# Performance work log

Hardware: AMD Instinct MI355X
Metric: run time of the kernel (lower is better)

## Reference

```python
import jax, jax.numpy as jnp
import numpy as np

BSZ, SEQ, NVARS = 4, 512, 7
DM, NH, DFF, EL, FACTOR, PRED = 512, 8, 2048, 2, 5, 96
DH = DM // NH


def layer_norm(x, g, b, eps=1e-5):
    mu = jnp.mean(x, -1, keepdims=True)
    var = jnp.mean((x - mu) ** 2, -1, keepdims=True)
    return (x - mu) / jnp.sqrt(var + eps) * g + b


def prob_attention(q, k, v, key, factor=FACTOR):
    # q,k,v: (B,H,L,D); Informer ProbSparse self-attention (non-causal)
    B, H, L, D = q.shape
    Lk = k.shape[2]
    U_part = min(int(factor * np.ceil(np.log(Lk))), Lk)  # sampled keys per query
    u = min(int(factor * np.ceil(np.log(L))), L)         # top queries kept
    idx = jax.random.randint(key, (L, U_part), 0, Lk)
    k_s = k[:, :, idx]                                   # (B,H,L,U,D) gathered keys
    qk_s = jnp.einsum('bhld,bhlud->bhlu', q, k_s)
    M = qk_s.max(-1) - qk_s.sum(-1) / Lk                 # sparsity measure (div by L_K, as in Informer)
    _, top = jax.lax.top_k(M, u)                         # (B,H,u) active query indices
    q_r = jnp.take_along_axis(q, top[..., None], axis=2)  # (B,H,u,D)
    scale = np.float32(1.0 / np.sqrt(D))
    scores = jnp.einsum('bhud,bhkd->bhuk', q_r, k) * scale
    attn = jax.nn.softmax(scores, axis=-1)
    upd = jnp.einsum('bhuk,bhkd->bhud', attn, v)
    # initial context = mean of V for every query; overwrite active queries
    ctx = jnp.broadcast_to(jnp.mean(v, axis=2, keepdims=True), (B, H, L, D))
    bi = jnp.arange(B)[:, None, None]
    hi = jnp.arange(H)[None, :, None]
    return ctx.at[bi, hi, top].set(upd)


def encoder_layer(x, p, key):
    Wq, bq, Wk, bk, Wv, bv, Wo, bo, W1, b1, W2, b2, g1, be1, g2, be2 = p
    B, L, _ = x.shape
    q = (x @ Wq.T + bq).reshape(B, L, NH, DH).transpose(0, 2, 1, 3)
    k = (x @ Wk.T + bk).reshape(B, L, NH, DH).transpose(0, 2, 1, 3)
    v = (x @ Wv.T + bv).reshape(B, L, NH, DH).transpose(0, 2, 1, 3)
    ctx = prob_attention(q, k, v, key)
    out = ctx.transpose(0, 2, 1, 3).reshape(B, L, DM) @ Wo.T + bo
    x = layer_norm(x + out, g1, be1)
    y = jax.nn.gelu(x @ W1.T + b1) @ W2.T + b2
    return layer_norm(x + y, g2, be2)


def _forward(x_enc, w_emb, b_emb, w_pos, Wq, bq, Wk, bk, Wv, bv, Wo, bo,
             W1, b1, W2, b2, g1, be1, g2, be2, gF, bF, Wh, bh):
    B, L, V = x_enc.shape
    emb = x_enc[..., None] * w_emb + b_emb               # (B,L,V,DM)  Linear(1,DM) per scalar
    h = emb.transpose(0, 2, 1, 3).reshape(B * V, L, DM) + w_pos
    base = jax.random.key(42)
    for l in range(EL):
        p = (Wq[l], bq[l], Wk[l], bk[l], Wv[l], bv[l], Wo[l], bo[l],
             W1[l], b1[l], W2[l], b2[l], g1[l], be1[l], g2[l], be2[l])
        h = encoder_layer(h, p, jax.random.fold_in(base, l))
    h = layer_norm(h, gF, bF)
    h = h.reshape(B, V, L * DM)                          # flatten head: nf = SEQ*DM
    out = h @ Wh.T + bh                                  # (B,V,PRED)
    return out.transpose(0, 2, 1)                        # (B,PRED,V)


def setup_inputs() -> dict:
    key = jax.random.key(0)
    ks = jax.random.split(key, 32)
    s = 0.02
    d = {
        'x_enc': jax.random.normal(ks[0], (BSZ, SEQ, NVARS), jnp.float32),
        'w_emb': jax.random.normal(ks[1], (DM,), jnp.float32) * s,
        'b_emb': jnp.zeros((DM,), jnp.float32),
        'w_pos': jax.random.normal(ks[2], (SEQ, DM), jnp.float32) * s,
        'Wq': jax.random.normal(ks[3], (EL, DM, DM), jnp.float32) * s,
        'bq': jnp.zeros((EL, DM), jnp.float32),
        'Wk': jax.random.normal(ks[4], (EL, DM, DM), jnp.float32) * s,
        'bk': jnp.zeros((EL, DM), jnp.float32),
        'Wv': jax.random.normal(ks[5], (EL, DM, DM), jnp.float32) * s,
        'bv': jnp.zeros((EL, DM), jnp.float32),
        'Wo': jax.random.normal(ks[6], (EL, DM, DM), jnp.float32) * s,
        'bo': jnp.zeros((EL, DM), jnp.float32),
        'W1': jax.random.normal(ks[7], (EL, DFF, DM), jnp.float32) * s,
        'b1': jnp.zeros((EL, DFF), jnp.float32),
        'W2': jax.random.normal(ks[8], (EL, DM, DFF), jnp.float32) * s,
        'b2': jnp.zeros((EL, DM), jnp.float32),
        'g1': jnp.ones((EL, DM), jnp.float32),
        'be1': jnp.zeros((EL, DM), jnp.float32),
        'g2': jnp.ones((EL, DM), jnp.float32),
        'be2': jnp.zeros((EL, DM), jnp.float32),
        'gF': jnp.ones((DM,), jnp.float32),
        'bF': jnp.zeros((DM,), jnp.float32),
        'Wh': jax.random.normal(ks[9], (PRED, SEQ * DM), jnp.float32) * 0.002,
        'bh': jnp.zeros((PRED,), jnp.float32),
    }
    return d


def reference(x_enc, w_emb, b_emb, w_pos, Wq, bq, Wk, bk, Wv, bv, Wo, bo,
              W1, b1, W2, b2, g1, be1, g2, be2, gF, bF, Wh, bh):
    return _forward(x_enc, w_emb, b_emb, w_pos, Wq, bq, Wk, bk, Wv, bv, Wo, bo,
                    W1, b1, W2, b2, g1, be1, g2, be2, gF, bF, Wh, bh)
```

## Files before the change

kernel.cpp:

```cpp
#include <hip/hip_runtime.h>
#include <math.h>

#define SEQL 512
#define DMOD 512
#define NHEAD 8
#define DHEAD 64
#define DFFN 2048
#define NBATCH 4
#define NVARS 7
#define NBV 28
#define NBH 224
#define NROWS 14336
#define NSAMP 35
#define NPRED 96
#define SBIG 7340032
#define QKS 1024

typedef short bf16x8 __attribute__((ext_vector_type(8)));
typedef float f32x4 __attribute__((ext_vector_type(4)));

#define GLDS(gptr, lptr) \
  __builtin_amdgcn_global_load_lds((const __attribute__((address_space(1))) void*)(gptr), \
                                   (__attribute__((address_space(3))) void*)(lptr), 16, 0, 0)

__device__ inline unsigned short f2b(float f) {
  unsigned u = __builtin_bit_cast(unsigned, f);
  unsigned r = (u + 0x7FFFu + ((u >> 16) & 1u)) >> 16;
  return (unsigned short)r;
}
__device__ inline float b2f(unsigned short h) {
  return __builtin_bit_cast(float, (unsigned)h << 16);
}

__device__ inline void threefry2x32(unsigned k0, unsigned k1,
                                    unsigned x0, unsigned x1,
                                    unsigned &o0, unsigned &o1) {
  unsigned ks2 = k0 ^ k1 ^ 0x1BD11BDAu;
  unsigned ks[3] = {k0, k1, ks2};
  x0 += k0; x1 += k1;
  const unsigned rot[2][4] = {{13u,15u,26u,6u},{17u,29u,16u,24u}};
  #pragma unroll
  for (int i = 0; i < 5; ++i) {
    #pragma unroll
    for (int j = 0; j < 4; ++j) {
      unsigned r = rot[i & 1][j];
      x0 += x1;
      x1 = (x1 << r) | (x1 >> (32u - r));
      x1 ^= x0;
    }
    x0 += ks[(i + 1) % 3];
    x1 += ks[(i + 2) % 3] + (unsigned)(i + 1);
  }
  o0 = x0; o1 = x1;
}

__global__ void make_idx_kernel(int layer, int* idx) {
  int i = blockIdx.x * 256 + threadIdx.x;
  if (i >= SEQL * NSAMP) return;
  unsigned kl0, kl1, o0, o1;
  threefry2x32(0u, 42u, 0u, (unsigned)layer, kl0, kl1);
  threefry2x32(kl0, kl1, (unsigned)i, (unsigned)(SEQL * NSAMP + i), o0, o1);
  idx[i] = (int)(o1 & 511u);
}

__global__ void embed_kernel(const float* __restrict__ x_enc,
                             const float* __restrict__ w_emb,
                             const float* __restrict__ b_emb,
                             const float* __restrict__ w_pos,
                             float* __restrict__ h,
                             unsigned short* __restrict__ h_hi,
                             unsigned short* __restrict__ h_lo) {
  size_t i = (size_t)blockIdx.x * 256 + threadIdx.x;
  if (i >= (size_t)(SBIG / 4)) return;
  size_t e = i * 4;
  int dm = (int)(e & 511);
  int l  = (int)((e >> 9) & 511);
  int bv = (int)(e >> 18);
  int b = bv / NVARS, v = bv % NVARS;
  float xs = x_enc[((size_t)b * SEQL + l) * NVARS + v];
  float4 we = *(const float4*)(w_emb + dm);
  float4 bb = *(const float4*)(b_emb + dm);
  float4 wp = *(const float4*)(w_pos + (size_t)l * DMOD + dm);
  float4 val;
  val.x = xs * we.x + bb.x + wp.x;
  val.y = xs * we.y + bb.y + wp.y;
  val.z = xs * we.z + bb.z + wp.z;
  val.w = xs * we.w + bb.w + wp.w;
  *(float4*)(h + e) = val;
  ushort4 hi4, lo4;
  hi4.x = f2b(val.x); lo4.x = f2b(val.x - b2f(hi4.x));
  hi4.y = f2b(val.y); lo4.y = f2b(val.y - b2f(hi4.y));
  hi4.z = f2b(val.z); lo4.z = f2b(val.z - b2f(hi4.z));
  hi4.w = f2b(val.w); lo4.w = f2b(val.w - b2f(hi4.w));
  *(ushort4*)(h_hi + e) = hi4;
  *(ushort4*)(h_lo + e) = lo4;
}

__global__ void prep_weights(const float* __restrict__ Wq, const float* __restrict__ Wk,
                             const float* __restrict__ Wv, const float* __restrict__ Wo,
                             const float* __restrict__ W1, const float* __restrict__ W2,
                             unsigned short* __restrict__ Wqk_hi, unsigned short* __restrict__ Wqk_lo,
                             unsigned short* __restrict__ Wv_b, unsigned short* __restrict__ Wo_b,
                             unsigned short* __restrict__ W1_b, unsigned short* __restrict__ W2_b) {
  const int Q4 = 65536;
  int g = blockIdx.x * 256 + threadIdx.x;
  if (g < 2 * Q4) {
    const float* src = g < Q4 ? Wq : Wk;
    unsigned short* hi = Wqk_hi + (g < Q4 ? 0 : DMOD * DMOD);
    unsigned short* lo = Wqk_lo + (g < Q4 ? 0 : DMOD * DMOD);
    int off = (g < Q4 ? g : g - Q4) * 4;
    float4 v = *(const float4*)(src + off);
    ushort4 h4, l4;
    h4.x = f2b(v.x); l4.x = f2b(v.x - b2f(h4.x));
    h4.y = f2b(v.y); l4.y = f2b(v.y - b2f(h4.y));
    h4.z = f2b(v.z); l4.z = f2b(v.z - b2f(h4.z));
    h4.w = f2b(v.w); l4.w = f2b(v.w - b2f(h4.w));
    *(ushort4*)(hi + off) = h4;
    *(ushort4*)(lo + off) = l4;
    return;
  }
  const float* src;
  unsigned short* dst;
  int off;
  if (g < 3 * Q4)      { src = Wv; dst = Wv_b; off = (g - 2 * Q4) * 4; }
  else if (g < 4 * Q4) { src = Wo; dst = Wo_b; off = (g - 3 * Q4) * 4; }
  else if (g < 4 * Q4 + 262144) { src = W1; dst = W1_b; off = (g - 4 * Q4) * 4; }
  else                 { src = W2; dst = W2_b; off = (g - 4 * Q4 - 262144) * 4; }
  float4 v = *(const float4*)(src + off);
  ushort4 o;
  o.x = f2b(v.x); o.y = f2b(v.y); o.z = f2b(v.z); o.w = f2b(v.w);
  *(ushort4*)(dst + off) = o;
}

__global__ __launch_bounds__(256) void gemm_mfma3(const unsigned short* __restrict__ Ah,
                                                  const unsigned short* __restrict__ Al,
                                                  const unsigned short* __restrict__ Bh,
                                                  const unsigned short* __restrict__ Bl,
                                                  const float* __restrict__ bq,
                                                  const float* __restrict__ bk,
                                                  float* __restrict__ C,
                                                  int M, int N, int K, int ldc) {
  __shared__ __align__(16) unsigned short AsH[128 * 64];
  __shared__ __align__(16) unsigned short AsL[128 * 64];
  __shared__ __align__(16) unsigned short BsH[128 * 64];
  __shared__ __align__(16) unsigned short BsL[128 * 64];
  int nwg = gridDim.x * gridDim.y;
  int flat = blockIdx.y * gridDim.x + blockIdx.x;
  int swz = (flat & 7) * (nwg >> 3) + (flat >> 3);
  int bxs = swz % gridDim.x, bys = swz / gridDim.x;
  int bm = bys * 128, bn = bxs * 128;
  int tid = threadIdx.x;
  int wave = tid >> 6, lane = tid & 63;
  int wr = wave >> 1, wc = wave & 1;
  int r16 = lane & 15, kq = lane >> 4;

  f32x4 acc[4][4];
  #pragma unroll
  for (int i = 0; i < 4; ++i)
    #pragma unroll
    for (int j = 0; j < 4; ++j) acc[i][j] = (f32x4){0.f, 0.f, 0.f, 0.f};

  for (int kt = 0; kt < K; kt += 64) {
    __syncthreads();
    #pragma unroll
    for (int i = 0; i < 4; ++i) {
      int c = i * 256 + tid;
      int row = c >> 3, kb = c & 7;
      int kbs = kb ^ (row & 7);
      size_t offA = (size_t)(bm + row) * K + kt + kbs * 8;
      size_t offB = (size_t)(bn + row) * K + kt + kbs * 8;
      int ldst = (i * 256 + (tid & 192)) << 4;
      GLDS(Ah + offA, (char*)AsH + ldst);
      GLDS(Al + offA, (char*)AsL + ldst);
      GLDS(Bh + offB, (char*)BsH + ldst);
      GLDS(Bl + offB, (char*)BsL + ldst);
    }
    __syncthreads();
    #pragma unroll
    for (int ks = 0; ks < 2; ++ks) {
      bf16x8 ah[4], al[4], bh[4], bl[4];
      #pragma unroll
      for (int mi = 0; mi < 4; ++mi) {
        int row = wr * 64 + mi * 16 + r16;
        int addr = ((row << 7) | (ks << 6) | (kq << 4)) ^ ((row & 7) << 4);
        ah[mi] = *(const bf16x8*)((const char*)AsH + addr);
        al[mi] = *(const bf16x8*)((const char*)AsL + addr);
      }
      #pragma unroll
      for (int ni = 0; ni < 4; ++ni) {
        int row = wc * 64 + ni * 16 + r16;
        int addr = ((row << 7) | (ks << 6) | (kq << 4)) ^ ((row & 7) << 4);
        bh[ni] = *(const bf16x8*)((const char*)BsH + addr);
        bl[ni] = *(const bf16x8*)((const char*)BsL + addr);
      }
      #pragma unroll
      for (int mi = 0; mi < 4; ++mi)
        #pragma unroll
        for (int ni = 0; ni < 4; ++ni) {
          acc[mi][ni] = __builtin_amdgcn_mfma_f32_16x16x32_bf16(ah[mi], bh[ni], acc[mi][ni], 0, 0, 0);
          acc[mi][ni] = __builtin_amdgcn_mfma_f32_16x16x32_bf16(ah[mi], bl[ni], acc[mi][ni], 0, 0, 0);
          acc[mi][ni] = __builtin_amdgcn_mfma_f32_16x16x32_bf16(al[mi], bh[ni], acc[mi][ni], 0, 0, 0);
        }
    }
  }
  int crow0 = bm + wr * 64 + (lane >> 4) * 4;
  int ccol0 = bn + wc * 64 + (lane & 15);
  #pragma unroll
  for (int mi = 0; mi < 4; ++mi) {
    #pragma unroll
    for (int ni = 0; ni < 4; ++ni) {
      int col = ccol0 + ni * 16;
      float bvv = col < 512 ? bq[col] : bk[col - 512];
      #pragma unroll
      for (int r = 0; r < 4; ++r) {
        int row = crow0 + mi * 16 + r;
        C[(size_t)row * ldc + col] = acc[mi][ni][r] + bvv;
      }
    }
  }
}

template<int ACT, int OUTBF>
__global__ __launch_bounds__(256) void gemm_mfma(const unsigned short* __restrict__ A,
                                                 const unsigned short* __restrict__ W,
                                                 const float* __restrict__ bias,
                                                 float* __restrict__ Cf,
                                                 unsigned short* __restrict__ Cb,
                                                 int M, int N, int K) {
  __shared__ __align__(16) unsigned short As[2][128 * 64];
  __shared__ __align__(16) unsigned short Bs[2][128 * 64];
  int nwg = gridDim.x * gridDim.y;
  int flat = blockIdx.y * gridDim.x + blockIdx.x;
  int swz = (flat & 7) * (nwg >> 3) + (flat >> 3);
  int bxs = swz % gridDim.x, bys = swz / gridDim.x;
  int bm = bys * 128, bn = bxs * 128;
  int tid = threadIdx.x;
  int wave = tid >> 6, lane = tid & 63;
  int wr = wave >> 1, wc = wave & 1;
  int r16 = lane & 15, kq = lane >> 4;

  f32x4 acc[4][4];
  #pragma unroll
  for (int i = 0; i < 4; ++i)
    #pragma unroll
    for (int j = 0; j < 4; ++j) acc[i][j] = (f32x4){0.f, 0.f, 0.f, 0.f};

#define STAGE_MM(buf, ktv) \
  { \
    for (int i_ = 0; i_ < 4; ++i_) { \
      int c_ = i_ * 256 + tid; \
      int row_ = c_ >> 3, kb_ = c_ & 7; \
      int kbs_ = kb_ ^ (row_ & 7); \
      size_t offA_ = (size_t)(bm + row_) * K + (ktv) + kbs_ * 8; \
      size_t offB_ = (size_t)(bn + row_) * K + (ktv) + kbs_ * 8; \
      int ldst_ = (i_ * 256 + (tid & 192)) << 4; \
      GLDS(A + offA_, (char*)As[buf] + ldst_); \
      GLDS(W + offB_, (char*)Bs[buf] + ldst_); \
    } \
  }

  int nkt = K >> 6;
  STAGE_MM(0, 0);
  __syncthreads();
  for (int t = 0; t < nkt; ++t) {
    int cur = t & 1;
    if (t + 1 < nkt) STAGE_MM(cur ^ 1, (t + 1) << 6);
    const char* Ab = (const char*)As[cur];
    const char* Bb = (const char*)Bs[cur];
    #pragma unroll
    for (int ks = 0; ks < 2; ++ks) {
      bf16x8 afr[4], bfr[4];
      #pragma unroll
      for (int mi = 0; mi < 4; ++mi) {
        int row = wr * 64 + mi * 16 + r16;
        int addr = ((row << 7) | (ks << 6) | (kq << 4)) ^ ((row & 7) << 4);
        afr[mi] = *(const bf16x8*)(Ab + addr);
      }
      #pragma unroll
      for (int ni = 0; ni < 4; ++ni) {
        int row = wc * 64 + ni * 16 + r16;
        int addr = ((row << 7) | (ks << 6) | (kq << 4)) ^ ((row & 7) << 4);
        bfr[ni] = *(const bf16x8*)(Bb + addr);
      }
      #pragma unroll
      for (int mi = 0; mi < 4; ++mi)
        #pragma unroll
        for (int ni = 0; ni < 4; ++ni)
          acc[mi][ni] = __builtin_amdgcn_mfma_f32_16x16x32_bf16(afr[mi], bfr[ni], acc[mi][ni], 0, 0, 0);
    }
    __syncthreads();
  }
#undef STAGE_MM

  int crow0 = bm + wr * 64 + (lane >> 4) * 4;
  int ccol0 = bn + wc * 64 + (lane & 15);
  #pragma unroll
  for (int mi = 0; mi < 4; ++mi) {
    #pragma unroll
    for (int ni = 0; ni < 4; ++ni) {
      int col = ccol0 + ni * 16;
      float bvv = bias[col];
      #pragma unroll
      for (int r = 0; r < 4; ++r) {
        int row = crow0 + mi * 16 + r;
        float v = acc[mi][ni][r] + bvv;
        if (ACT) {
          float x = v;
          float u = x * __builtin_fmaf(0.044715f * x, x, 1.0f);
          float tme = __expf(-1.5957691216057308f * u);
          v = x * __builtin_amdgcn_rcpf(1.0f + tme);
        }
        if (OUTBF) Cb[(size_t)row * N + col] = f2b(v);
        else       Cf[(size_t)row * N + col] = v;
      }
    }
  }
}

__global__ __launch_bounds__(512) void m2_kernel(const float* __restrict__ QK,
                                                 const int* __restrict__ idx,
                                                 float* __restrict__ Mout) {
  int bh = blockIdx.x;
  int bv = bh >> 3, head = bh & 7;
  int tid = threadIdx.x;
  __shared__ float Ks[512 * 64];
  const float* base = QK + (size_t)bv * (SEQL * QKS);
  for (int c = tid; c < 512 * 16; c += 512) {
    int l = c >> 4, db = c & 15;
    float4 v = *(const float4*)(base + (size_t)l * QKS + 512 + head * 64 + db * 4);
    *(float4*)(Ks + l * 64 + ((db ^ (l & 15)) << 2)) = v;
  }
  float q[64];
  const float* qp = base + (size_t)tid * QKS + head * 64;
  #pragma unroll
  for (int d4 = 0; d4 < 64; d4 += 4) {
    float4 qv = *(const float4*)(qp + d4);
    q[d4 + 0] = qv.x; q[d4 + 1] = qv.y; q[d4 + 2] = qv.z; q[d4 + 3] = qv.w;
  }
  __syncthreads();
  const int* ip = idx + tid * NSAMP;
  float mx = -INFINITY, sm = 0.f;
  for (int u = 0; u < NSAMP; ++u) {
    int kidx = ip[u];
    const float* kr = Ks + kidx * 64;
    int x = kidx & 15;
    float s = 0.f;
    #pragma unroll
    for (int db = 0; db < 16; ++db) {
      float4 kv = *(const float4*)(kr + ((db ^ x) << 2));
      s += q[db * 4 + 0] * kv.x + q[db * 4 + 1] * kv.y
         + q[db * 4 + 2] * kv.z + q[db * 4 + 3] * kv.w;
    }
    mx = fmaxf(mx, s);
    sm += s;
  }
  Mout[(size_t)bh * SEQL + tid] = mx - sm * (1.0f / 512.0f);
}

__global__ __launch_bounds__(256) void topk_kernel(const float* __restrict__ Mv,
                                                   int* __restrict__ top) {
  int bh = blockIdx.x;
  int tid = threadIdx.x;
  __shared__ float vals[512];
  __shared__ float rv[256];
  __shared__ int ri[256];
  vals[tid]       = Mv[(size_t)bh * SEQL + tid];
  vals[tid + 256] = Mv[(size_t)bh * SEQL + tid + 256];
  __syncthreads();
  for (int t = 0; t < NSAMP; ++t) {
    float v0 = vals[tid], v1 = vals[tid + 256];
    float bvv; int bii;
    if (v0 >= v1) { bvv = v0; bii = tid; } else { bvv = v1; bii = tid + 256; }
    rv[tid] = bvv; ri[tid] = bii;
    __syncthreads();
    for (int s = 128; s > 0; s >>= 1) {
      if (tid < s) {
        float ov = rv[tid + s]; int oi = ri[tid + s];
        if (ov > rv[tid] || (ov == rv[tid] && oi < ri[tid])) { rv[tid] = ov; ri[tid] = oi; }
      }
      __syncthreads();
    }
    if (tid == 0) { top[bh * NSAMP + t] = ri[0]; vals[ri[0]] = -INFINITY; }
    __syncthreads();
  }
}

__global__ __launch_bounds__(256) void vmean_kernel(const unsigned short* __restrict__ Vb,
                                                    float* __restrict__ vmean) {
  int bv = blockIdx.x;
  int t = threadIdx.x;
  const unsigned short* vb = Vb + (size_t)bv * (SEQL * DMOD) + t * 2;
  float s0 = 0.f, s1 = 0.f;
  #pragma unroll 4
  for (int l = 0; l < SEQL; ++l) {
    unsigned u = *(const unsigned*)(vb + (size_t)l * DMOD);
    s0 += b2f((unsigned short)(u & 0xffffu));
// ... 87 lines not shown
      for (int j = 0; j < 8; ++j) {
        int l = (wv * 8 + j) * 16 + r16;
        #pragma unroll
        for (int r = 0; r < 4; ++r) {
          int u = m * 16 + kq * 4 + r;
          int byte = ((u << 10) | (l << 1)) ^ ((u & 7) << 4);
          *(unsigned short*)((char*)P + byte) = f2b(acc[m][j][r]);
        }
      }
  }
  __syncthreads();

  for (int c = tid; c < 512 * 8; c += 256) {
    int l = c >> 3, dq = c & 7;
    bf16x8 v8 = *(const bf16x8*)(vbase + (size_t)l * DMOD + dq * 8);
    #pragma unroll
    for (int j = 0; j < 8; ++j) {
      int d = dq * 8 + j;
      int byte = ((d << 10) | (l << 1)) ^ ((d & 7) << 4);
      *(unsigned short*)((char*)KV + byte) = (unsigned short)v8[j];
    }
  }
  for (int u = wv; u < NSAMP; u += 4) {
    int byte = ((u << 10) | (lane << 4)) ^ ((u & 7) << 4);
    bf16x8 sv = *(const bf16x8*)((const char*)P + byte);
    float s[8];
    #pragma unroll
    for (int j = 0; j < 8; ++j) s[j] = b2f((unsigned short)sv[j]);
    float mx = s[0];
    #pragma unroll
    for (int j = 1; j < 8; ++j) mx = fmaxf(mx, s[j]);
    #pragma unroll
    for (int off = 32; off > 0; off >>= 1) mx = fmaxf(mx, __shfl_xor(mx, off));
    float e[8], sm = 0.f;
    #pragma unroll
    for (int j = 0; j < 8; ++j) { e[j] = __expf(s[j] - mx); sm += e[j]; }
    #pragma unroll
    for (int off = 32; off > 0; off >>= 1) sm += __shfl_xor(sm, off);
    float inv = 1.0f / sm;
    bf16x8 pv;
    #pragma unroll
    for (int j = 0; j < 8; ++j) pv[j] = (short)f2b(e[j] * inv);
    *(bf16x8*)((char*)P + byte) = pv;
  }
  __syncthreads();

  {
    f32x4 acc2[3];
    #pragma unroll
    for (int m = 0; m < 3; ++m) acc2[m] = (f32x4){0.f, 0.f, 0.f, 0.f};
    for (int kst = 0; kst < 16; ++kst) {
      int vrow = wv * 16 + r16;
      int baddr = ((vrow << 10) | (kst << 6) | (kq << 4)) ^ ((vrow & 7) << 4);
      bf16x8 bfr = *(const bf16x8*)((const char*)KV + baddr);
      #pragma unroll
      for (int m = 0; m < 3; ++m) {
        int prow = m * 16 + r16;
        int aaddr = ((prow << 10) | (kst << 6) | (kq << 4)) ^ ((prow & 7) << 4);
        bf16x8 afr2 = *(const bf16x8*)((const char*)P + aaddr);
        acc2[m] = __builtin_amdgcn_mfma_f32_16x16x32_bf16(afr2, bfr, acc2[m], 0, 0, 0);
      }
    }
    int d = wv * 16 + r16;
    #pragma unroll
    for (int m = 0; m < 3; ++m)
      #pragma unroll
      for (int r = 0; r < 4; ++r) {
        int u = m * 16 + kq * 4 + r;
        if (u < NSAMP) {
          size_t off = (size_t)bv * (SEQL * DMOD) + (size_t)topi[u] * DMOD + head * 64 + d;
          ctxb[off] = f2b(acc2[m][r]);
        }
      }
  }
}

template<int BMODE, int OUT>
__global__ __launch_bounds__(256) void add_ln(const float* __restrict__ a,
                                              const unsigned short* __restrict__ b,
                                              const float* __restrict__ g,
                                              const float* __restrict__ be,
                                              float* __restrict__ out,
                                              unsigned short* __restrict__ outb,
                                              unsigned short* __restrict__ outh,
                                              unsigned short* __restrict__ outl) {
  int row = blockIdx.x * 2 + (threadIdx.x >> 7);
  int t = threadIdx.x & 127;
  int wave = threadIdx.x >> 6;
  int lane = threadIdx.x & 63;
  size_t base = (size_t)row * DMOD + t * 4;
  float4 x = *(const float4*)(a + base);
  if (BMODE == 2) {
    ushort4 r4 = *(const ushort4*)(b + base);
    x.x += b2f(r4.x); x.y += b2f(r4.y); x.z += b2f(r4.z); x.w += b2f(r4.w);
  }
  float s1 = x.x + x.y + x.z + x.w;
  float s2 = x.x * x.x + x.y * x.y + x.z * x.z + x.w * x.w;
  #pragma unroll
  for (int off = 32; off > 0; off >>= 1) {
    s1 += __shfl_xor(s1, off);
    s2 += __shfl_xor(s2, off);
  }
  __shared__ float sh[8];
  if (lane == 0) { sh[wave * 2] = s1; sh[wave * 2 + 1] = s2; }
  __syncthreads();
  int mate = wave ^ 1;
  s1 += sh[mate * 2];
  s2 += sh[mate * 2 + 1];
  float mu = s1 * (1.0f / 512.0f);
  float var = s2 * (1.0f / 512.0f) - mu * mu;
  float rstd = rsqrtf(var + 1e-5f);
  float4 gg = *(const float4*)(g + t * 4);
  float4 bb = *(const float4*)(be + t * 4);
  float4 o;
  o.x = (x.x - mu) * rstd * gg.x + bb.x;
  o.y = (x.y - mu) * rstd * gg.y + bb.y;
  o.z = (x.z - mu) * rstd * gg.z + bb.z;
  o.w = (x.w - mu) * rstd * gg.w + bb.w;
  *(float4*)(out + base) = o;
  if (OUT == 1) {
    ushort4 ob;
    ob.x = f2b(o.x); ob.y = f2b(o.y); ob.z = f2b(o.z); ob.w = f2b(o.w);
    *(ushort4*)(outb + base) = ob;
  }
  if (OUT == 2) {
    ushort4 hi4, lo4;
    hi4.x = f2b(o.x); lo4.x = f2b(o.x - b2f(hi4.x));
    hi4.y = f2b(o.y); lo4.y = f2b(o.y - b2f(hi4.y));
    hi4.z = f2b(o.z); lo4.z = f2b(o.z - b2f(hi4.z));
    hi4.w = f2b(o.w); lo4.w = f2b(o.w - b2f(hi4.w));
    *(ushort4*)(outh + base) = hi4;
    *(ushort4*)(outl + base) = lo4;
  }
}

__global__ __launch_bounds__(256) void head_partial_mfma(const unsigned short* __restrict__ hbf,
                                                         const float* __restrict__ Wh,
                                                         float* __restrict__ partial) {
  __shared__ __align__(16) unsigned short Hs[32 * 512];
  __shared__ __align__(16) unsigned short Ws[96 * 512];
  int blk = blockIdx.x;
  int k0 = blk * 512;
  int tid = threadIdx.x;
  int wv = tid >> 6, lane = tid & 63;
  int r16 = lane & 15, kq = lane >> 4;

  for (int c = tid; c < 32 * 64; c += 256) {
    int row = c >> 6, col8 = c & 63;
    int src = row < 28 ? row : 0;
    bf16x8 v = *(const bf16x8*)(hbf + (size_t)src * 262144 + k0 + col8 * 8);
    int byte = ((row << 10) | (col8 << 4)) ^ ((row & 7) << 4);
    *(bf16x8*)((char*)Hs + byte) = v;
  }
  for (int c = tid; c < 96 * 64; c += 256) {
    int row = c >> 6, col8 = c & 63;
    const float* src = Wh + (size_t)row * 262144 + k0 + col8 * 8;
    float4 va = *(const float4*)(src);
    float4 vb = *(const float4*)(src + 4);
    bf16x8 o8;
    o8[0] = (short)f2b(va.x); o8[1] = (short)f2b(va.y);
    o8[2] = (short)f2b(va.z); o8[3] = (short)f2b(va.w);
    o8[4] = (short)f2b(vb.x); o8[5] = (short)f2b(vb.y);
    o8[6] = (short)f2b(vb.z); o8[7] = (short)f2b(vb.w);
    int byte = ((row << 10) | (col8 << 4)) ^ ((row & 7) << 4);
    *(bf16x8*)((char*)Ws + byte) = o8;
  }
  __syncthreads();

  f32x4 acc[2][6];
  #pragma unroll
  for (int mt = 0; mt < 2; ++mt)
    #pragma unroll
    for (int nt = 0; nt < 6; ++nt) acc[mt][nt] = (f32x4){0.f, 0.f, 0.f, 0.f};

  #pragma unroll
  for (int kk = 0; kk < 4; ++kk) {
    int kfrag = wv * 4 + kk;
    bf16x8 afr[2];
    #pragma unroll
    for (int mt = 0; mt < 2; ++mt) {
      int row = mt * 16 + r16;
      int byte = ((row << 10) | (kfrag << 6) | (kq << 4)) ^ ((row & 7) << 4);
      afr[mt] = *(const bf16x8*)((const char*)Hs + byte);
    }
    #pragma unroll
    for (int nt = 0; nt < 6; ++nt) {
      int row = nt * 16 + r16;
      int byte = ((row << 10) | (kfrag << 6) | (kq << 4)) ^ ((row & 7) << 4);
      bf16x8 bfr = *(const bf16x8*)((const char*)Ws + byte);
      #pragma unroll
      for (int mt = 0; mt < 2; ++mt)
        acc[mt][nt] = __builtin_amdgcn_mfma_f32_16x16x32_bf16(afr[mt], bfr, acc[mt][nt], 0, 0, 0);
    }
  }
  size_t prow = (size_t)(blk * 4 + wv) * 2688;
  #pragma unroll
  for (int mt = 0; mt < 2; ++mt)
    #pragma unroll
    for (int nt = 0; nt < 6; ++nt)
      #pragma unroll
      for (int r = 0; r < 4; ++r) {
        int m = mt * 16 + kq * 4 + r;
        int n = nt * 16 + r16;
        if (m < 28) partial[prow + m * 96 + n] = acc[mt][nt][r];
      }
}

__global__ __launch_bounds__(256) void head_reduce(const float* __restrict__ partial,
                                                   const float* __restrict__ bh_,
                                                   float* __restrict__ out) {
  int o = blockIdx.x;
  int tid = threadIdx.x;
  float s = 0.f;
  for (int b = tid; b < 2048; b += 256) s += partial[(size_t)b * 2688 + o];
  __shared__ float red[256];
  red[tid] = s;
  __syncthreads();
  for (int st = 128; st > 0; st >>= 1) {
    if (tid < st) red[tid] += red[tid + st];
    __syncthreads();
  }
  if (tid == 0) {
    int m = o / 96, p = o % 96;
    int b = m / NVARS, v = m % NVARS;
    out[(size_t)b * (NPRED * NVARS) + (size_t)p * NVARS + v] = red[0] + bh_[p];
  }
}

extern "C" void kernel_launch(void* const* d_in, const int* in_sizes, int n_in,
                              void* d_out, int out_size, void* d_ws, size_t ws_size,
                              hipStream_t stream) {
  const float* x_enc = (const float*)d_in[0];
  const float* w_emb = (const float*)d_in[1];
  const float* b_emb = (const float*)d_in[2];
  const float* w_pos = (const float*)d_in[3];
  const float* Wq = (const float*)d_in[4];
  const float* bq = (const float*)d_in[5];
  const float* Wk = (const float*)d_in[6];
  const float* bk = (const float*)d_in[7];
  const float* Wv = (const float*)d_in[8];
  const float* bv_ = (const float*)d_in[9];
  const float* Wo = (const float*)d_in[10];
  const float* bo = (const float*)d_in[11];
  const float* W1 = (const float*)d_in[12];
  const float* b1 = (const float*)d_in[13];
  const float* W2 = (const float*)d_in[14];
  const float* b2 = (const float*)d_in[15];
  const float* g1 = (const float*)d_in[16];
  const float* be1 = (const float*)d_in[17];
  const float* g2 = (const float*)d_in[18];
  const float* be2 = (const float*)d_in[19];
  const float* gF = (const float*)d_in[20];
  const float* bF = (const float*)d_in[21];
  const float* Wh = (const float*)d_in[22];
  const float* bh_ = (const float*)d_in[23];
  float* out = (float*)d_out;

  const size_t S = (size_t)SBIG;
  const size_t SB = S * 4;
  char* ws = (char*)d_ws;
  float* h    = (float*)(ws);
  float* QKb  = (float*)(ws + SB);
  unsigned short* Vb   = (unsigned short*)(ws + 3 * SB);
  unsigned short* Ob_b = (unsigned short*)(ws + 3 * SB + SB / 2);
  unsigned short* Wqk_hi = (unsigned short*)(ws + 4 * SB);
  unsigned short* Wqk_lo = (unsigned short*)(ws + 4 * SB + 0x100000);
  unsigned short* Wv_b = (unsigned short*)(ws + 4 * SB + 0x200000);
  unsigned short* Wo_b = (unsigned short*)(ws + 4 * SB + 0x280000);
  unsigned short* W1_b = (unsigned short*)(ws + 4 * SB + 0x300000);
  unsigned short* W2_b = (unsigned short*)(ws + 4 * SB + 0x500000);
  unsigned short* h_hi = (unsigned short*)(ws + 5 * SB);
  unsigned short* h_lo = (unsigned short*)(ws + 5 * SB + SB / 2);
  unsigned short* CTXb = h_hi;
  unsigned short* h_bf = h_lo;
  unsigned short* FFNb = (unsigned short*)QKb;
  float* partial = QKb;
  int*   idx = (int*)(ws + 6 * SB);
  float* Mv  = (float*)(ws + 6 * SB + 0x20000);
  int*   top = (int*)(ws + 6 * SB + 0xA0000);
  float* vmean = (float*)(ws + 6 * SB + 0xB0000);
  if (ws_size < 6 * SB + 0xC0000) return;

  dim3 b256(256);
  int gVec = (int)(S / 4 / 256);

  embed_kernel<<<gVec, b256, 0, stream>>>(x_enc, w_emb, b_emb, w_pos, h, h_hi, h_lo);

  for (int l = 0; l < 2; ++l) {
    const float* Wql = Wq + (size_t)l * DMOD * DMOD;
    const float* Wkl = Wk + (size_t)l * DMOD * DMOD;
    const float* Wvl = Wv + (size_t)l * DMOD * DMOD;
    const float* Wol = Wo + (size_t)l * DMOD * DMOD;
    const float* W1l = W1 + (size_t)l * DFFN * DMOD;
    const float* W2l = W2 + (size_t)l * DMOD * DFFN;

    prep_weights<<<3072, b256, 0, stream>>>(Wql, Wkl, Wvl, Wol, W1l, W2l,
                                            Wqk_hi, Wqk_lo, Wv_b, Wo_b, W1_b, W2_b);

    dim3 gqk(QKS / 128, NROWS / 128);
    gemm_mfma3<<<gqk, b256, 0, stream>>>(h_hi, h_lo, Wqk_hi, Wqk_lo,
                                         bq + l * DMOD, bk + l * DMOD,
                                         QKb, NROWS, QKS, DMOD, QKS);
    dim3 gv(DMOD / 128, NROWS / 128);
    gemm_mfma<0, 1><<<gv, b256, 0, stream>>>(h_hi, Wv_b, bv_ + l * DMOD,
                                             (float*)0, Vb, NROWS, DMOD, DMOD);

    make_idx_kernel<<<(SEQL * NSAMP + 255) / 256, b256, 0, stream>>>(l, idx);
    m2_kernel<<<NBH, dim3(512), 0, stream>>>(QKb, idx, Mv);
    topk_kernel<<<NBH, b256, 0, stream>>>(Mv, top);
    vmean_kernel<<<NBV, b256, 0, stream>>>(Vb, vmean);
    ctx_fill_kernel<<<gVec, b256, 0, stream>>>(vmean, CTXb);
    attn2_kernel<<<NBH, b256, 0, stream>>>(QKb, Vb, top, CTXb);

    dim3 go(DMOD / 128, NROWS / 128);
    gemm_mfma<0, 1><<<go, b256, 0, stream>>>(CTXb, Wo_b, bo + l * DMOD,
                                             (float*)0, Ob_b, NROWS, DMOD, DMOD);
    add_ln<2, 1><<<NROWS / 2, b256, 0, stream>>>(h, Ob_b, g1 + l * DMOD, be1 + l * DMOD,
                                                 h, h_bf, (unsigned short*)0, (unsigned short*)0);

    dim3 gf1(DFFN / 128, NROWS / 128);
    gemm_mfma<1, 1><<<gf1, b256, 0, stream>>>(h_bf, W1_b, b1 + l * DFFN,
                                              (float*)0, FFNb, NROWS, DFFN, DMOD);
    dim3 gf2(DMOD / 128, NROWS / 128);
    gemm_mfma<0, 1><<<gf2, b256, 0, stream>>>(FFNb, W2_b, b2 + l * DMOD,
                                              (float*)0, Ob_b, NROWS, DMOD, DFFN);
    if (l == 0) {
      add_ln<2, 2><<<NROWS / 2, b256, 0, stream>>>(h, Ob_b, g2 + l * DMOD, be2 + l * DMOD,
                                                   h, (unsigned short*)0, h_hi, h_lo);
    } else {
      add_ln<2, 0><<<NROWS / 2, b256, 0, stream>>>(h, Ob_b, g2 + l * DMOD, be2 + l * DMOD,
                                                   h, (unsigned short*)0, (unsigned short*)0, (unsigned short*)0);
    }
  }

  add_ln<0, 1><<<NROWS / 2, b256, 0, stream>>>(h, (const unsigned short*)0, gF, bF,
                                               h, h_bf, (unsigned short*)0, (unsigned short*)0);
  head_partial_mfma<<<512, b256, 0, stream>>>(h_bf, Wh, partial);
  head_reduce<<<NBV * NPRED, b256, 0, stream>>>(partial, bh_, out);
}
```

Before: 754.3 us.

## Double-buffer split-bf16 GEMM with K=32 stages and k-major LDS layout

```diff
diff --git a/kernel.cpp b/kernel.cpp
--- a/kernel.cpp
+++ b/kernel.cpp
@@ -140,10 +140,10 @@
                                                   const float* __restrict__ bk,
                                                   float* __restrict__ C,
                                                   int M, int N, int K, int ldc) {
-  __shared__ __align__(16) unsigned short AsH[128 * 64];
-  __shared__ __align__(16) unsigned short AsL[128 * 64];
-  __shared__ __align__(16) unsigned short BsH[128 * 64];
-  __shared__ __align__(16) unsigned short BsL[128 * 64];
+  __shared__ __align__(16) unsigned short AsH[2][128 * 32];
+  __shared__ __align__(16) unsigned short AsL[2][128 * 32];
+  __shared__ __align__(16) unsigned short BsH[2][128 * 32];
+  __shared__ __align__(16) unsigned short BsL[2][128 * 32];
   int nwg = gridDim.x * gridDim.y;
   int flat = blockIdx.y * gridDim.x + blockIdx.x;
   int swz = (flat & 7) * (nwg >> 3) + (flat >> 3);
@@ -160,49 +160,58 @@
     #pragma unroll
     for (int j = 0; j < 4; ++j) acc[i][j] = (f32x4){0.f, 0.f, 0.f, 0.f};
 
-  for (int kt = 0; kt < K; kt += 64) {
+#define STAGE_M3(buf, ktv) \
+  { \
+    for (int i_ = 0; i_ < 2; ++i_) { \
+      int c_ = i_ * 256 + tid; \
+      int kq_ = c_ >> 7, row_ = c_ & 127; \
+      size_t offA_ = (size_t)(bm + row_) * K + (ktv) + kq_ * 8; \
+      size_t offB_ = (size_t)(bn + row_) * K + (ktv) + kq_ * 8; \
+      int ldst_ = (i_ * 256 + (tid & 192)) << 4; \
+      GLDS(Ah + offA_, (char*)AsH[buf] + ldst_); \
+      GLDS(Al + offA_, (char*)AsL[buf] + ldst_); \
+      GLDS(Bh + offB_, (char*)BsH[buf] + ldst_); \
+      GLDS(Bl + offB_, (char*)BsL[buf] + ldst_); \
+    } \
+  }
+
+  int nkt = K >> 5;
+  STAGE_M3(0, 0);
+  __syncthreads();
+  for (int t = 0; t < nkt; ++t) {
+    int cur = t & 1;
+    if (t + 1 < nkt) STAGE_M3(cur ^ 1, (t + 1) << 5);
+    const char* AbH = (const char*)AsH[cur];
+    const char* AbL = (const char*)AsL[cur];
+    const char* BbH = (const char*)BsH[cur];
+    const char* BbL = (const char*)BsL[cur];
+    bf16x8 ah[4], al[4], bh[4], bl[4];
+    #pragma unroll
+    for (int mi = 0; mi < 4; ++mi) {
+      int row = wr * 64 + mi * 16 + r16;
+      int addr = (kq << 11) | (row << 4);
+      ah[mi] = *(const bf16x8*)(AbH + addr);
+      al[mi] = *(const bf16x8*)(AbL + addr);
+    }
+    #pragma unroll
+    for (int ni = 0; ni < 4; ++ni) {
+      int row = wc * 64 + ni * 16 + r16;
+      int addr = (kq << 11) | (row << 4);
+      bh[ni] = *(const bf16x8*)(BbH + addr);
+      bl[ni] = *(const bf16x8*)(BbL + addr);
+    }
+    #pragma unroll
+    for (int mi = 0; mi < 4; ++mi)
+      #pragma unroll
+      for (int ni = 0; ni < 4; ++ni) {
+        acc[mi][ni] = __builtin_amdgcn_mfma_f32_16x16x32_bf16(ah[mi], bh[ni], acc[mi][ni], 0, 0, 0);
+        acc[mi][ni] = __builtin_amdgcn_mfma_f32_16x16x32_bf16(ah[mi], bl[ni], acc[mi][ni], 0, 0, 0);
+        acc[mi][ni] = __builtin_amdgcn_mfma_f32_16x16x32_bf16(al[mi], bh[ni], acc[mi][ni], 0, 0, 0);
+      }
     __syncthreads();
-    #pragma unroll
-    for (int i = 0; i < 4; ++i) {
-      int c = i * 256 + tid;
-      int row = c >> 3, kb = c & 7;
-      int kbs = kb ^ (row & 7);
-      size_t offA = (size_t)(bm + row) * K + kt + kbs * 8;
-      size_t offB = (size_t)(bn + row) * K + kt + kbs * 8;
-      int ldst = (i * 256 + (tid & 192)) << 4;
-      GLDS(Ah + offA, (char*)AsH + ldst);
-      GLDS(Al + offA, (char*)AsL + ldst);
-      GLDS(Bh + offB, (char*)BsH + ldst);
-      GLDS(Bl + offB, (char*)BsL + ldst);
-    }
-    __syncthreads();
-    #pragma unroll
-    for (int ks = 0; ks < 2; ++ks) {
-      bf16x8 ah[4], al[4], bh[4], bl[4];
-      #pragma unroll
-      for (int mi = 0; mi < 4; ++mi) {
-        int row = wr * 64 + mi * 16 + r16;
-        int addr = ((row << 7) | (ks << 6) | (kq << 4)) ^ ((row & 7) << 4);
-        ah[mi] = *(const bf16x8*)((const char*)AsH + addr);
-        al[mi] = *(const bf16x8*)((const char*)AsL + addr);
-      }
-      #pragma unroll
-      for (int ni = 0; ni < 4; ++ni) {
-        int row = wc * 64 + ni * 16 + r16;
-        int addr = ((row << 7) | (ks << 6) | (kq << 4)) ^ ((row & 7) << 4);
-        bh[ni] = *(const bf16x8*)((const char*)BsH + addr);
-        bl[ni] = *(const bf16x8*)((const char*)BsL + addr);
-      }
-      #pragma unroll
-      for (int mi = 0; mi < 4; ++mi)
-        #pragma unroll
-        for (int ni = 0; ni < 4; ++ni) {
-          acc[mi][ni] = __builtin_amdgcn_mfma_f32_16x16x32_bf16(ah[mi], bh[ni], acc[mi][ni], 0, 0, 0);
-          acc[mi][ni] = __builtin_amdgcn_mfma_f32_16x16x32_bf16(ah[mi], bl[ni], acc[mi][ni], 0, 0, 0);
-          acc[mi][ni] = __builtin_amdgcn_mfma_f32_16x16x32_bf16(al[mi], bh[ni], acc[mi][ni], 0, 0, 0);
-        }
-    }
-  }
+  }
+#undef STAGE_M3
+
   int crow0 = bm + wr * 64 + (lane >> 4) * 4;
   int ccol0 = bn + wc * 64 + (lane & 15);
   #pragma unroll
@@ -249,10 +258,9 @@
   { \
     for (int i_ = 0; i_ < 4; ++i_) { \
       int c_ = i_ * 256 + tid; \
-      int row_ = c_ >> 3, kb_ = c_ & 7; \
-      int kbs_ = kb_ ^ (row_ & 7); \
-      size_t offA_ = (size_t)(bm + row_) * K + (ktv) + kbs_ * 8; \
-      size_t offB_ = (size_t)(bn + row_) * K + (ktv) + kbs_ * 8; \
+      int ks_ = c_ >> 9, kq_ = (c_ >> 7) & 3, row_ = c_ & 127; \
+      size_t offA_ = (size_t)(bm + row_) * K + (ktv) + ks_ * 32 + kq_ * 8; \
+      size_t offB_ = (size_t)(bn + row_) * K + (ktv) + ks_ * 32 + kq_ * 8; \
       int ldst_ = (i_ * 256 + (tid & 192)) << 4; \
       GLDS(A + offA_, (char*)As[buf] + ldst_); \
       GLDS(W + offB_, (char*)Bs[buf] + ldst_); \
@@ -273,13 +281,13 @@
       #pragma unroll
       for (int mi = 0; mi < 4; ++mi) {
         int row = wr * 64 + mi * 16 + r16;
-        int addr = ((row << 7) | (ks << 6) | (kq << 4)) ^ ((row & 7) << 4);
+        int addr = (ks << 13) | (kq << 11) | (row << 4);
         afr[mi] = *(const bf16x8*)(Ab + addr);
       }
       #pragma unroll
       for (int ni = 0; ni < 4; ++ni) {
         int row = wc * 64 + ni * 16 + r16;
-        int addr = ((row << 7) | (ks << 6) | (kq << 4)) ^ ((row & 7) << 4);
+        int addr = (ks << 13) | (kq << 11) | (row << 4);
         bfr[ni] = *(const bf16x8*)(Bb + addr);
       }
       #pragma unroll
```

New measurement: 1.020 ms. 1.35x slower.

## Fold split-bf16 QK GEMM into single double-buffered GEMM via concatenated K

Applied to the files above, without the earlier changes.

```diff
diff --git a/kernel.cpp b/kernel.cpp
--- a/kernel.cpp
+++ b/kernel.cpp
@@ -15,6 +15,7 @@
 #define NPRED 96
 #define SBIG 7340032
 #define QKS 1024
+#define K3 1536
 
 typedef short bf16x8 __attribute__((ext_vector_type(8)));
 typedef float f32x4 __attribute__((ext_vector_type(4)));
@@ -68,8 +69,7 @@
                              const float* __restrict__ b_emb,
                              const float* __restrict__ w_pos,
                              float* __restrict__ h,
-                             unsigned short* __restrict__ h_hi,
-                             unsigned short* __restrict__ h_lo) {
+                             unsigned short* __restrict__ h3) {
   size_t i = (size_t)blockIdx.x * 256 + threadIdx.x;
   if (i >= (size_t)(SBIG / 4)) return;
   size_t e = i * 4;
@@ -92,141 +92,68 @@
   hi4.y = f2b(val.y); lo4.y = f2b(val.y - b2f(hi4.y));
   hi4.z = f2b(val.z); lo4.z = f2b(val.z - b2f(hi4.z));
   hi4.w = f2b(val.w); lo4.w = f2b(val.w - b2f(hi4.w));
-  *(ushort4*)(h_hi + e) = hi4;
-  *(ushort4*)(h_lo + e) = lo4;
+  size_t row = e >> 9;
+  size_t base3 = row * K3 + (e & 511);
+  *(ushort4*)(h3 + base3)        = hi4;
+  *(ushort4*)(h3 + base3 + 512)  = hi4;
+  *(ushort4*)(h3 + base3 + 1024) = lo4;
 }
 
 __global__ void prep_weights(const float* __restrict__ Wq, const float* __restrict__ Wk,
                              const float* __restrict__ Wv, const float* __restrict__ Wo,
                              const float* __restrict__ W1, const float* __restrict__ W2,
-                             unsigned short* __restrict__ Wqk_hi, unsigned short* __restrict__ Wqk_lo,
+                             const float* __restrict__ bq, const float* __restrict__ bk,
+                             unsigned short* __restrict__ Wqk3,
                              unsigned short* __restrict__ Wv_b, unsigned short* __restrict__ Wo_b,
-                             unsigned short* __restrict__ W1_b, unsigned short* __restrict__ W2_b) {
-  const int Q4 = 65536;
+                             unsigned short* __restrict__ W1_b, unsigned short* __restrict__ W2_b,
+                             float* __restrict__ bias_qk) {
   int g = blockIdx.x * 256 + threadIdx.x;
-  if (g < 2 * Q4) {
-    const float* src = g < Q4 ? Wq : Wk;
-    unsigned short* hi = Wqk_hi + (g < Q4 ? 0 : DMOD * DMOD);
-    unsigned short* lo = Wqk_lo + (g < Q4 ? 0 : DMOD * DMOD);
-    int off = (g < Q4 ? g : g - Q4) * 4;
-    float4 v = *(const float4*)(src + off);
-    ushort4 h4, l4;
-    h4.x = f2b(v.x); l4.x = f2b(v.x - b2f(h4.x));
-    h4.y = f2b(v.y); l4.y = f2b(v.y - b2f(h4.y));
-    h4.z = f2b(v.z); l4.z = f2b(v.z - b2f(h4.z));
-    h4.w = f2b(v.w); l4.w = f2b(v.w - b2f(h4.w));
-    *(ushort4*)(hi + off) = h4;
-    *(ushort4*)(lo + off) = l4;
+  const int NQK = 1024 * K3 / 4;
+  if (g < NQK) {
+    int n = g / 384, cg = g % 384;
+    const float* w = n < 512 ? Wq + (size_t)n * 512 : Wk + (size_t)(n - 512) * 512;
+    int lo_mode, sc4;
+    if (cg < 128)      { lo_mode = 0; sc4 = cg; }
+    else if (cg < 256) { lo_mode = 1; sc4 = cg - 128; }
+    else               { lo_mode = 0; sc4 = cg - 256; }
+    float4 v = *(const float4*)(w + sc4 * 4);
+    ushort4 o;
+    if (lo_mode) {
+      unsigned short hx = f2b(v.x), hy = f2b(v.y), hz = f2b(v.z), hw = f2b(v.w);
+      o.x = f2b(v.x - b2f(hx)); o.y = f2b(v.y - b2f(hy));
+      o.z = f2b(v.z - b2f(hz)); o.w = f2b(v.w - b2f(hw));
+    } else {
+      o.x = f2b(v.x); o.y = f2b(v.y); o.z = f2b(v.z); o.w = f2b(v.w);
+    }
+    *(ushort4*)(Wqk3 + (size_t)n * K3 + cg * 4) = o;
     return;
   }
+  g -= NQK;
   const float* src;
   unsigned short* dst;
-  int off;
-  if (g < 3 * Q4)      { src = Wv; dst = Wv_b; off = (g - 2 * Q4) * 4; }
-  else if (g < 4 * Q4) { src = Wo; dst = Wo_b; off = (g - 3 * Q4) * 4; }
-  else if (g < 4 * Q4 + 262144) { src = W1; dst = W1_b; off = (g - 4 * Q4) * 4; }
-  else                 { src = W2; dst = W2_b; off = (g - 4 * Q4 - 262144) * 4; }
+  if (g < 65536)        { src = Wv; dst = Wv_b; }
+  else if (g < 131072)  { src = Wo; dst = Wo_b; g -= 65536; }
+  else if (g < 393216)  { src = W1; dst = W1_b; g -= 131072; }
+  else if (g < 655360)  { src = W2; dst = W2_b; g -= 393216; }
+  else {
+    int i = g - 655360;
+    if (i < 1024) bias_qk[i] = i < 512 ? bq[i] : bk[i - 512];
+    return;
+  }
+  int off = g * 4;
   float4 v = *(const float4*)(src + off);
   ushort4 o;
   o.x = f2b(v.x); o.y = f2b(v.y); o.z = f2b(v.z); o.w = f2b(v.w);
   *(ushort4*)(dst + off) = o;
 }
 
-__global__ __launch_bounds__(256) void gemm_mfma3(const unsigned short* __restrict__ Ah,
-                                                  const unsigned short* __restrict__ Al,
-                                                  const unsigned short* __restrict__ Bh,
-                                                  const unsigned short* __restrict__ Bl,
-                                                  const float* __restrict__ bq,
-                                                  const float* __restrict__ bk,
-                                                  float* __restrict__ C,
-                                                  int M, int N, int K, int ldc) {
-  __shared__ __align__(16) unsigned short AsH[128 * 64];
-  __shared__ __align__(16) unsigned short AsL[128 * 64];
-  __shared__ __align__(16) unsigned short BsH[128 * 64];
-  __shared__ __align__(16) unsigned short BsL[128 * 64];
-  int nwg = gridDim.x * gridDim.y;
-  int flat = blockIdx.y * gridDim.x + blockIdx.x;
-  int swz = (flat & 7) * (nwg >> 3) + (flat >> 3);
-  int bxs = swz % gridDim.x, bys = swz / gridDim.x;
-  int bm = bys * 128, bn = bxs * 128;
-  int tid = threadIdx.x;
-  int wave = tid >> 6, lane = tid & 63;
-  int wr = wave >> 1, wc = wave & 1;
-  int r16 = lane & 15, kq = lane >> 4;
-
-  f32x4 acc[4][4];
-  #pragma unroll
-  for (int i = 0; i < 4; ++i)
-    #pragma unroll
-    for (int j = 0; j < 4; ++j) acc[i][j] = (f32x4){0.f, 0.f, 0.f, 0.f};
-
-  for (int kt = 0; kt < K; kt += 64) {
-    __syncthreads();
-    #pragma unroll
-    for (int i = 0; i < 4; ++i) {
-      int c = i * 256 + tid;
-      int row = c >> 3, kb = c & 7;
-      int kbs = kb ^ (row & 7);
-      size_t offA = (size_t)(bm + row) * K + kt + kbs * 8;
-      size_t offB = (size_t)(bn + row) * K + kt + kbs * 8;
-      int ldst = (i * 256 + (tid & 192)) << 4;
-      GLDS(Ah + offA, (char*)AsH + ldst);
-      GLDS(Al + offA, (char*)AsL + ldst);
-      GLDS(Bh + offB, (char*)BsH + ldst);
-      GLDS(Bl + offB, (char*)BsL + ldst);
-    }
-    __syncthreads();
-    #pragma unroll
-    for (int ks = 0; ks < 2; ++ks) {
-      bf16x8 ah[4], al[4], bh[4], bl[4];
-      #pragma unroll
-      for (int mi = 0; mi < 4; ++mi) {
-        int row = wr * 64 + mi * 16 + r16;
-        int addr = ((row << 7) | (ks << 6) | (kq << 4)) ^ ((row & 7) << 4);
-        ah[mi] = *(const bf16x8*)((const char*)AsH + addr);
-        al[mi] = *(const bf16x8*)((const char*)AsL + addr);
-      }
-      #pragma unroll
-      for (int ni = 0; ni < 4; ++ni) {
-        int row = wc * 64 + ni * 16 + r16;
-        int addr = ((row << 7) | (ks << 6) | (kq << 4)) ^ ((row & 7) << 4);
-        bh[ni] = *(const bf16x8*)((const char*)BsH + addr);
-        bl[ni] = *(const bf16x8*)((const char*)BsL + addr);
-      }
-      #pragma unroll
-      for (int mi = 0; mi < 4; ++mi)
-        #pragma unroll
-        for (int ni = 0; ni < 4; ++ni) {
-          acc[mi][ni] = __builtin_amdgcn_mfma_f32_16x16x32_bf16(ah[mi], bh[ni], acc[mi][ni], 0, 0, 0);
-          acc[mi][ni] = __builtin_amdgcn_mfma_f32_16x16x32_bf16(ah[mi], bl[ni], acc[mi][ni], 0, 0, 0);
-          acc[mi][ni] = __builtin_amdgcn_mfma_f32_16x16x32_bf16(al[mi], bh[ni], acc[mi][ni], 0, 0, 0);
-        }
-    }
-  }
-  int crow0 = bm + wr * 64 + (lane >> 4) * 4;
-  int ccol0 = bn + wc * 64 + (lane & 15);
-  #pragma unroll
-  for (int mi = 0; mi < 4; ++mi) {
-    #pragma unroll
-    for (int ni = 0; ni < 4; ++ni) {
-      int col = ccol0 + ni * 16;
-      float bvv = col < 512 ? bq[col] : bk[col - 512];
-      #pragma unroll
-      for (int r = 0; r < 4; ++r) {
-        int row = crow0 + mi * 16 + r;
-        C[(size_t)row * ldc + col] = acc[mi][ni][r] + bvv;
-      }
-    }
-  }
-}
-
 template<int ACT, int OUTBF>
-__global__ __launch_bounds__(256) void gemm_mfma(const unsigned short* __restrict__ A,
-                                                 const unsigned short* __restrict__ W,
+__global__ __launch_bounds__(256) void gemm_mfma(const unsigned short* __restrict__ A, int lda,
+                                                 const unsigned short* __restrict__ W, int ldb,
                                                  const float* __restrict__ bias,
                                                  float* __restrict__ Cf,
                                                  unsigned short* __restrict__ Cb,
-                                                 int M, int N, int K) {
+                                                 int M, int N, int K, int ldc) {
   __shared__ __align__(16) unsigned short As[2][128 * 64];
   __shared__ __align__(16) unsigned short Bs[2][128 * 64];
   int nwg = gridDim.x * gridDim.y;
@@ -251,8 +178,8 @@
       int c_ = i_ * 256 + tid; \
       int row_ = c_ >> 3, kb_ = c_ & 7; \
       int kbs_ = kb_ ^ (row_ & 7); \
-      size_t offA_ = (size_t)(bm + row_) * K + (ktv) + kbs_ * 8; \
-      size_t offB_ = (size_t)(bn + row_) * K + (ktv) + kbs_ * 8; \
+      size_t offA_ = (size_t)(bm + row_) * lda + (ktv) + kbs_ * 8; \
+      size_t offB_ = (size_t)(bn + row_) * ldb + (ktv) + kbs_ * 8; \
       int ldst_ = (i_ * 256 + (tid & 192)) << 4; \
       GLDS(A + offA_, (char*)As[buf] + ldst_); \
       GLDS(W + offB_, (char*)Bs[buf] + ldst_); \
@@ -310,8 +237,8 @@
           float tme = __expf(-1.5957691216057308f * u);
           v = x * __builtin_amdgcn_rcpf(1.0f + tme);
         }
-        if (OUTBF) Cb[(size_t)row * N + col] = f2b(v);
-        else       Cf[(size_t)row * N + col] = v;
+        if (OUTBF) Cb[(size_t)row * ldc + col] = f2b(v);
+        else       Cf[(size_t)row * ldc + col] = v;
       }
     }
   }
@@ -565,8 +492,7 @@
                                               const float* __restrict__ be,
                                               float* __restrict__ out,
                                               unsigned short* __restrict__ outb,
-                                              unsigned short* __restrict__ outh,
-                                              unsigned short* __restrict__ outl) {
+                                              unsigned short* __restrict__ outh3) {
   int row = blockIdx.x * 2 + (threadIdx.x >> 7);
   int t = threadIdx.x & 127;
   int wave = threadIdx.x >> 6;
@@ -606,14 +532,16 @@
     ob.x = f2b(o.x); ob.y = f2b(o.y); ob.z = f2b(o.z); ob.w = f2b(o.w);
     *(ushort4*)(outb + base) = ob;
   }
-  if (OUT == 2) {
+  if (OUT == 3) {
     ushort4 hi4, lo4;
     hi4.x = f2b(o.x); lo4.x = f2b(o.x - b2f(hi4.x));
     hi4.y = f2b(o.y); lo4.y = f2b(o.y - b2f(hi4.y));
     hi4.z = f2b(o.z); lo4.z = f2b(o.z - b2f(hi4.z));
     hi4.w = f2b(o.w); lo4.w = f2b(o.w - b2f(hi4.w));
-    *(ushort4*)(outh + base) = hi4;
-    *(ushort4*)(outl + base) = lo4;
+    size_t base3 = (size_t)row * K3 + t * 4;
+    *(ushort4*)(outh3 + base3)        = hi4;
+    *(ushort4*)(outh3 + base3 + 512)  = hi4;
+    *(ushort4*)(outh3 + base3 + 1024) = lo4;
   }
 }
 
@@ -746,16 +674,15 @@
   float* QKb  = (float*)(ws + SB);
   unsigned short* Vb   = (unsigned short*)(ws + 3 * SB);
   unsigned short* Ob_b = (unsigned short*)(ws + 3 * SB + SB / 2);
-  unsigned short* Wqk_hi = (unsigned short*)(ws + 4 * SB);
-  unsigned short* Wqk_lo = (unsigned short*)(ws + 4 * SB + 0x100000);
-  unsigned short* Wv_b = (unsigned short*)(ws + 4 * SB + 0x200000);
-  unsigned short* Wo_b = (unsigned short*)(ws + 4 * SB + 0x280000);
-  unsigned short* W1_b = (unsigned short*)(ws + 4 * SB + 0x300000);
-  unsigned short* W2_b = (unsigned short*)(ws + 4 * SB + 0x500000);
-  unsigned short* h_hi = (unsigned short*)(ws + 5 * SB);
-  unsigned short* h_lo = (unsigned short*)(ws + 5 * SB + SB / 2);
-  unsigned short* CTXb = h_hi;
-  unsigned short* h_bf = h_lo;
+  unsigned short* Wqk3 = (unsigned short*)(ws + 4 * SB);
+  unsigned short* Wv_b = (unsigned short*)(ws + 4 * SB + 0x300000);
+  unsigned short* Wo_b = (unsigned short*)(ws + 4 * SB + 0x380000);
+  unsigned short* W1_b = (unsigned short*)(ws + 4 * SB + 0x400000);
+  unsigned short* W2_b = (unsigned short*)(ws + 4 * SB + 0x600000);
+  float* bias_qk       = (float*)(ws + 4 * SB + 0x800000);
+  unsigned short* h3 = (unsigned short*)(ws + 4 * SB + 0x900000);
+  unsigned short* CTXb = h3;
+  unsigned short* h_bf = (unsigned short*)((char*)h3 + 0x1000000);
   unsigned short* FFNb = (unsigned short*)QKb;
   float* partial = QKb;
   int*   idx = (int*)(ws + 6 * SB);
@@ -767,7 +694,7 @@
   dim3 b256(256);
   int gVec = (int)(S / 4 / 256);
 
-  embed_kernel<<<gVec, b256, 0, stream>>>(x_enc, w_emb, b_emb, w_pos, h, h_hi, h_lo);
+  embed_kernel<<<gVec, b256, 0, stream>>>(x_enc, w_emb, b_emb, w_pos, h, h3);
 
   for (int l = 0; l < 2; ++l) {
     const float* Wql = Wq + (size_t)l * DMOD * DMOD;
@@ -777,16 +704,17 @@
     const float* W1l = W1 + (size_t)l * DFFN * DMOD;
     const float* W2l = W2 + (size_t)l * DMOD * DFFN;
 
-    prep_weights<<<3072, b256, 0, stream>>>(Wql, Wkl, Wvl, Wol, W1l, W2l,
-                                            Wqk_hi, Wqk_lo, Wv_b, Wo_b, W1_b, W2_b);
+    prep_weights<<<4100, b256, 0, stream>>>(Wql, Wkl, Wvl, Wol, W1l, W2l,
+                                            bq + l * DMOD, bk + l * DMOD,
+                                            Wqk3, Wv_b, Wo_b, W1_b, W2_b, bias_qk);
 
     dim3 gqk(QKS / 128, NROWS / 128);
-    gemm_mfma3<<<gqk, b256, 0, stream>>>(h_hi, h_lo, Wqk_hi, Wqk_lo,
-                                         bq + l * DMOD, bk + l * DMOD,
-                                         QKb, NROWS, QKS, DMOD, QKS);
+    gemm_mfma<0, 0><<<gqk, b256, 0, stream>>>(h3, K3, Wqk3, K3, bias_qk,
+                                              QKb, (unsigned short*)0,
+                                              NROWS, QKS, K3, QKS);
     dim3 gv(DMOD / 128, NROWS / 128);
-    gemm_mfma<0, 1><<<gv, b256, 0, stream>>>(h_hi, Wv_b, bv_ + l * DMOD,
-                                             (float*)0, Vb, NROWS, DMOD, DMOD);
+    gemm_mfma<0, 1><<<gv, b256, 0, stream>>>(h3, K3, Wv_b, DMOD, bv_ + l * DMOD,
+                                             (float*)0, Vb, NROWS, DMOD, DMOD, DMOD);
 
     make_idx_kernel<<<(SEQL * NSAMP + 255) / 256, b256, 0, stream>>>(l, idx);
     m2_kernel<<<NBH, dim3(512), 0, stream>>>(QKb, idx, Mv);
@@ -796,28 +724,28 @@
     attn2_kernel<<<NBH, b256, 0, stream>>>(QKb, Vb, top, CTXb);
 
     dim3 go(DMOD / 128, NROWS / 128);
-    gemm_mfma<0, 1><<<go, b256, 0, stream>>>(CTXb, Wo_b, bo + l * DMOD,
-                                             (float*)0, Ob_b, NROWS, DMOD, DMOD);
+    gemm_mfma<0, 1><<<go, b256, 0, stream>>>(CTXb, DMOD, Wo_b, DMOD, bo + l * DMOD,
+                                             (float*)0, Ob_b, NROWS, DMOD, DMOD, DMOD);
     add_ln<2, 1><<<NROWS / 2, b256, 0, stream>>>(h, Ob_b, g1 + l * DMOD, be1 + l * DMOD,
-                                                 h, h_bf, (unsigned short*)0, (unsigned short*)0);
+                                                 h, h_bf, (unsigned short*)0);
 
     dim3 gf1(DFFN / 128, NROWS / 128);
-    gemm_mfma<1, 1><<<gf1, b256, 0, stream>>>(h_bf, W1_b, b1 + l * DFFN,
-                                              (float*)0, FFNb, NROWS, DFFN, DMOD);
+    gemm_mfma<1, 1><<<gf1, b256, 0, stream>>>(h_bf, DMOD, W1_b, DMOD, b1 + l * DFFN,
+                                              (float*)0, FFNb, NROWS, DFFN, DMOD, DFFN);
     dim3 gf2(DMOD / 128, NROWS / 128);
-    gemm_mfma<0, 1><<<gf2, b256, 0, stream>>>(FFNb, W2_b, b2 + l * DMOD,
-                                              (float*)0, Ob_b, NROWS, DMOD, DFFN);
+    gemm_mfma<0, 1><<<gf2, b256, 0, stream>>>(FFNb, DFFN, W2_b, DFFN, b2 + l * DMOD,
+                                              (float*)0, Ob_b, NROWS, DMOD, DFFN, DMOD);
     if (l == 0) {
-      add_ln<2, 2><<<NROWS / 2, b256, 0, stream>>>(h, Ob_b, g2 + l * DMOD, be2 + l * DMOD,
-                                                   h, (unsigned short*)0, h_hi, h_lo);
+      add_ln<2, 3><<<NROWS / 2, b256, 0, stream>>>(h, Ob_b, g2 + l * DMOD, be2 + l * DMOD,
+                                                   h, (unsigned short*)0, h3);
     } else {
       add_ln<2, 0><<<NROWS / 2, b256, 0, stream>>>(h, Ob_b, g2 + l * DMOD, be2 + l * DMOD,
-                                                   h, (unsigned short*)0, (unsigned short*)0, (unsigned short*)0);
+                                                   h, (unsigned short*)0, (unsigned short*)0);
     }
   }
 
   add_ln<0, 1><<<NROWS / 2, b256, 0, stream>>>(h, (const unsigned short*)0, gF, bF,
-                                               h, h_bf, (unsigned short*)0, (unsigned short*)0);
+                                               h, h_bf, (unsigned short*)0);
   head_partial_mfma<<<512, b256, 0, stream>>>(h_bf, Wh, partial);
   head_reduce<<<NBV * NPRED, b256, 0, stream>>>(partial, bh_, out);
 }
```

After: 803.7 us. +6.6%, slower.
